# Kernel tuning notes

Hardware: AMD Instinct MI355X
Metric: run time of the kernel (lower is better)

## Reference

```python
import jax, jax.numpy as jnp
import numpy as np

H = 16  # num_heads
LN_EPS = 1e-5


def setup_inputs() -> dict:
    key = jax.random.key(0)
    ks = jax.random.split(key, 12)
    B, S, HS = 2, 1024, 1024
    D = HS // H
    vocab = 2 * 512 + 1  # 2*max_relative_position + 1
    inp = {
        "q": jax.random.normal(ks[0], (B, S, HS), jnp.float32),
        "k": jax.random.normal(ks[1], (B, S, HS), jnp.float32),
        "v": jax.random.normal(ks[2], (B, S, HS), jnp.float32),
        "rel_positions": jax.random.randint(ks[3], (S, S), 0, vocab, jnp.int64),
        "Wq": jax.random.normal(ks[4], (HS, HS), jnp.float32) * 0.02,
        "bq": jnp.zeros((HS,), jnp.float32),
        "Wk": jax.random.normal(ks[5], (HS, HS), jnp.float32) * 0.02,
        "bk": jnp.zeros((HS,), jnp.float32),
        "Wv": jax.random.normal(ks[6], (HS, HS), jnp.float32) * 0.02,
        "bv": jnp.zeros((HS,), jnp.float32),
        "rel_key_emb": jax.random.normal(ks[7], (vocab, D), jnp.float32) * 0.02,
        "rel_val_emb": jax.random.normal(ks[8], (vocab, D), jnp.float32) * 0.02,
        "Wo": jax.random.normal(ks[9], (HS, HS), jnp.float32) * 0.02,
        "bo": jnp.zeros((HS,), jnp.float32),
        "ln_g": jnp.ones((HS,), jnp.float32),
        "ln_b": jnp.zeros((HS,), jnp.float32),
    }
    return inp


def _layer_norm(x, g, b):
    mu = jnp.mean(x, axis=-1, keepdims=True)
    var = jnp.mean(jnp.square(x - mu), axis=-1, keepdims=True)
    return (x - mu) * jax.lax.rsqrt(var + LN_EPS) * g + b


def reference(q, k, v, rel_positions, Wq, bq, Wk, bk, Wv, bv,
              rel_key_emb, rel_val_emb, Wo, bo, ln_g, ln_b):
    B, S, HS = q.shape
    D = HS // H
    residual = q
    # projections (torch Linear: x @ W^T + b), split heads -> (B,H,S,D)
    qh = (q @ Wq.T + bq).reshape(B, S, H, D).transpose(0, 2, 1, 3)
    kh = (k @ Wk.T + bk).reshape(B, S, H, D).transpose(0, 2, 1, 3)
    vh = (v @ Wv.T + bv).reshape(B, S, H, D).transpose(0, 2, 1, 3)
    # relative embeddings: (S,S,D)
    rk = rel_key_emb[rel_positions]
    rv = rel_val_emb[rel_positions]
    # logits: content + relative-key term (note: original has NO 1/sqrt(d) scaling)
    logits = jnp.einsum('bhqd,bhkd->bhqk', qh, kh) \
           + jnp.einsum('bhqd,qkd->bhqk', qh, rk)
    weights = jax.nn.softmax(logits, axis=-1)
    # output: content + relative-value term
    ctx = jnp.einsum('bhqk,bhkd->bhqd', weights, vh) \
        + jnp.einsum('bhqk,qkd->bhqd', weights, rv)
    out = ctx.transpose(0, 2, 1, 3).reshape(B, S, HS) @ Wo.T + bo
    out = _layer_norm(out + residual, ln_g, ln_b)
    return (out, weights)
```

## Files before the change

kernel.cpp:

```cpp
#include <hip/hip_runtime.h>
#include <hip/hip_bf16.h>
#include <stdint.h>

#define B_   2
#define S_   1024
#define HS_  1024
#define H_   16
#define D_   64
#define V_   1025
#define VP_  1056
#define BH_  32
#define RTS_S 1072
#define RVS_  66

typedef __attribute__((ext_vector_type(8))) short  short8;
typedef __attribute__((ext_vector_type(4))) short  short4v;
typedef __attribute__((ext_vector_type(4))) float  floatx4;
typedef __attribute__((ext_vector_type(4))) int    intx4;
typedef __bf16 bf16x8 __attribute__((ext_vector_type(8)));

__device__ inline short f2b(float f) {
  union { float f; uint32_t u; } c; c.f = f;
  uint32_t u = c.u;
  uint32_t r = (u + 0x7fffu + ((u >> 16) & 1u)) >> 16;
  return (short)r;
}
__device__ inline float b2f(short s) {
  union { uint32_t u; float f; } c; c.u = ((uint32_t)(uint16_t)s) << 16;
  return c.f;
}
__device__ inline short8 cvt8(const float* p) {
  const floatx4* p4 = reinterpret_cast<const floatx4*>(p);
  floatx4 x = p4[0], y = p4[1];
  short8 r;
  r[0]=f2b(x[0]); r[1]=f2b(x[1]); r[2]=f2b(x[2]); r[3]=f2b(x[3]);
  r[4]=f2b(y[0]); r[5]=f2b(y[1]); r[6]=f2b(y[2]); r[7]=f2b(y[3]);
  return r;
}
__device__ inline short8 load_s8(const short* p) {
  return *reinterpret_cast<const short8*>(p);
}
__device__ inline floatx4 mfma16(short8 a, short8 b, floatx4 c) {
  return __builtin_amdgcn_mfma_f32_16x16x32_bf16(
      __builtin_bit_cast(bf16x8, a), __builtin_bit_cast(bf16x8, b), c, 0, 0, 0);
}

__global__ __launch_bounds__(256) void k_prep(const float* __restrict__ rve,
                                              const float* __restrict__ rke,
                                              short* __restrict__ rveB,
                                              short* __restrict__ rkeB) {
  int idx = blockIdx.x * 256 + threadIdx.x;
  if (idx < V_ * D_) {
    rveB[idx] = f2b(rve[idx]);
  } else {
    int j = idx - V_ * D_;
    if (j < V_ * D_) rkeB[j] = f2b(rke[j]);
  }
}

__global__ __launch_bounds__(256) void k_cvt(
    const float* __restrict__ q, const float* __restrict__ k, const float* __restrict__ v,
    const float* __restrict__ Wq, const float* __restrict__ Wk,
    const float* __restrict__ Wv, const float* __restrict__ Wo,
    short* __restrict__ xb, short* __restrict__ wb) {
  int z = blockIdx.z;
  const float* src = z == 0 ? q : z == 1 ? k : z == 2 ? v
                   : z == 3 ? Wq : z == 4 ? Wk : z == 5 ? Wv : Wo;
  int n = (z < 3) ? (1 << 21) : (1 << 20);
  short* dst = (z < 3) ? xb + (size_t)z * (1 << 21) : wb + (size_t)(z - 3) * (1 << 20);
  int i = (blockIdx.x * 256 + threadIdx.x) * 8;
  if (i < n) *reinterpret_cast<short8*>(&dst[i]) = cvt8(src + i);
}


__global__ __launch_bounds__(256, 4) void k_proj(
    const short* __restrict__ xb, const short* __restrict__ wb,
    const float* __restrict__ bq, const float* __restrict__ bk, const float* __restrict__ bv,
    short* __restrict__ qh, short* __restrict__ kh, short* __restrict__ vhT) {
  int which = blockIdx.z;
  const short* A  = xb + (size_t)which * (2048u * 1024u);
  const short* Bm = wb + (size_t)which * (1024u * 1024u);
  const float* bias = which == 0 ? bq : which == 1 ? bk : bv;
  int m0 = blockIdx.x * 64, n0 = blockIdx.y * 64;
  int tid = threadIdx.x, wid = tid >> 6, lane = tid & 63;
  int wr = wid >> 1, wc = wid & 1, qd = lane >> 4, c16 = lane & 15;
  __shared__ short As[4 * 64 * 8];
  __shared__ short Bs[4 * 64 * 8];
  int kk = tid & 3, rowi = tid >> 2;
  const short* ga = A  + (size_t)(m0 + rowi) * HS_ + kk * 8;
  const short* gb = Bm + (size_t)(n0 + rowi) * HS_ + kk * 8;
  floatx4 acc[2][2] = {};
  for (int k0 = 0; k0 < HS_; k0 += 32) {
    short8 av = load_s8(ga + k0);
    short8 bv8 = load_s8(gb + k0);
    __syncthreads();
    *reinterpret_cast<short8*>(&As[kk * 512 + rowi * 8]) = av;
    *reinterpret_cast<short8*>(&Bs[kk * 512 + rowi * 8]) = bv8;
    __syncthreads();
    short8 a0 = load_s8(&As[qd * 512 + (wr * 32 + c16) * 8]);
    short8 a1 = load_s8(&As[qd * 512 + (wr * 32 + 16 + c16) * 8]);
    short8 b0 = load_s8(&Bs[qd * 512 + (wc * 32 + c16) * 8]);
    short8 b1 = load_s8(&Bs[qd * 512 + (wc * 32 + 16 + c16) * 8]);
    acc[0][0] = mfma16(a0, b0, acc[0][0]);
    acc[0][1] = mfma16(a0, b1, acc[0][1]);
    acc[1][0] = mfma16(a1, b0, acc[1][0]);
    acc[1][1] = mfma16(a1, b1, acc[1][1]);
  }
#pragma unroll
  for (int mi = 0; mi < 2; mi++)
#pragma unroll
    for (int ni = 0; ni < 2; ni++) {
      int col = n0 + wc * 32 + ni * 16 + c16;
      float bs = bias[col];
      int gr0 = m0 + wr * 32 + mi * 16 + qd * 4;
      if (which < 2) {
        short* dst = which == 0 ? qh : kh;
#pragma unroll
        for (int r = 0; r < 4; r++)
          dst[(size_t)(gr0 + r) * HS_ + col] = f2b(acc[mi][ni][r] + bs);
      } else {
        int h = col >> 6, d = col & 63;
        int bb = gr0 >> 10, s = gr0 & 1023;
        short4v pk;
#pragma unroll
        for (int r = 0; r < 4; r++) pk[r] = f2b(acc[mi][ni][r] + bs);
        *reinterpret_cast<short4v*>(&vhT[(((size_t)(bb * H_ + h)) * D_ + d) * S_ + s]) = pk;
      }
    }
}

__global__ __launch_bounds__(256, 4) void k_score(
    const short* __restrict__ qh, const short* __restrict__ kh,
    const short* __restrict__ rkeB, const int* __restrict__ rp,
    float* __restrict__ weights) {
  int bh = blockIdx.y;
  int b = bh >> 4, h = bh & 15;
  int q0 = blockIdx.x * 16;
  int tid = threadIdx.x, wave = tid >> 6, lane = tid & 63;
  int qd = lane >> 4, c16 = lane & 15;
  __shared__ short Rt[16 * RTS_S];
  __shared__ float redA[4 * 16];
  __shared__ float redB[4 * 16];

  const short* aptr = qh + ((size_t)b * S_ + q0 + c16) * HS_ + h * 64 + qd * 8;
  short8 a0 = load_s8(aptr), a1 = load_s8(aptr + 32);

  for (int nt = wave; nt < VP_ / 16; nt += 4) {
    int p = nt * 16 + c16;
    short8 b0 = {}, b1 = {};
    if (p < V_) {
      b0 = load_s8(rkeB + (size_t)p * D_ + qd * 8);
      b1 = load_s8(rkeB + (size_t)p * D_ + 32 + qd * 8);
    }
    floatx4 acc = {};
    acc = mfma16(a0, b0, acc);
    acc = mfma16(a1, b1, acc);
#pragma unroll
    for (int r = 0; r < 4; r++) Rt[(qd * 4 + r) * RTS_S + p] = f2b(acc[r]);
  }
  __syncthreads();

  floatx4 acc[16];
  const int* rpq = rp + (size_t)q0 * S_;
#pragma unroll
  for (int it = 0; it < 16; it++) {
    int col = wave * 256 + it * 16 + c16;
    const short* bptr = kh + ((size_t)b * S_ + col) * HS_ + h * 64 + qd * 8;
    floatx4 a = {};
    a = mfma16(a0, load_s8(bptr), a);
    a = mfma16(a1, load_s8(bptr + 32), a);
#pragma unroll
    for (int r = 0; r < 4; r++) {
      int row = qd * 4 + r;
      int p = rpq[(size_t)row * S_ + col];
      a[r] += b2f(Rt[row * RTS_S + p]);
    }
    acc[it] = a;
  }

  float mx[4], inv[4];
#pragma unroll
  for (int r = 0; r < 4; r++) {
    float m = -1e30f;
#pragma unroll
    for (int it = 0; it < 16; it++) m = fmaxf(m, acc[it][r]);
#pragma unroll
    for (int off = 1; off < 16; off <<= 1) m = fmaxf(m, __shfl_xor(m, off));
    mx[r] = m;
    if (c16 == 0) redA[wave * 16 + qd * 4 + r] = m;
  }
  __syncthreads();
#pragma unroll
  for (int r = 0; r < 4; r++) {
    int row = qd * 4 + r;
    float m = fmaxf(fmaxf(redA[row], redA[16 + row]),
                    fmaxf(redA[32 + row], redA[48 + row]));
    mx[r] = m;
  }
  float sm[4] = {0.f, 0.f, 0.f, 0.f};
#pragma unroll
  for (int it = 0; it < 16; it++) {
#pragma unroll
    for (int r = 0; r < 4; r++) {
      float e = __expf(acc[it][r] - mx[r]);
      acc[it][r] = e;
      sm[r] += e;
    }
  }
#pragma unroll
  for (int r = 0; r < 4; r++) {
#pragma unroll
    for (int off = 1; off < 16; off <<= 1) sm[r] += __shfl_xor(sm[r], off);
    if (c16 == 0) redB[wave * 16 + qd * 4 + r] = sm[r];
  }
  __syncthreads();
#pragma unroll
  for (int r = 0; r < 4; r++) {
    int row = qd * 4 + r;
    inv[r] = 1.f / (redB[row] + redB[16 + row] + redB[32 + row] + redB[48 + row]);
  }

  float* wout = weights + (size_t)bh * S_ * S_ + (size_t)q0 * S_;
#pragma unroll
  for (int it = 0; it < 16; it++) {
    int col = wave * 256 + it * 16 + c16;
#pragma unroll
    for (int r = 0; r < 4; r++) {
      wout[(size_t)(qd * 4 + r) * S_ + col] = acc[it][r] * inv[r];
    }
  }
}

__global__ __launch_bounds__(256, 4) void k_relgemm(
    const float* __restrict__ weights, const int* __restrict__ rp,
    const short* __restrict__ rveB, float* __restrict__ ctx_rel) {
  int q = blockIdx.x;
  int tid = threadIdx.x, wave = tid >> 6, lane = tid & 63;
  int qd = lane >> 4, c16 = lane & 15;
  __shared__ int   rpl[S_];
  __shared__ short Wl[32][40];
  __shared__ short Rv[32][RVS_];

  {
    const intx4* r4 = reinterpret_cast<const intx4*>(rp + (size_t)q * S_);
    reinterpret_cast<intx4*>(rpl)[tid] = r4[tid];
  }
  __syncthreads();

  int sn = tid >> 3;
  int sk = (tid & 3) * 8;
  int part = tid & 7;
  const float* wbase = weights + ((size_t)sn * S_ + q) * S_;
  floatx4 acc0 = {}, acc1 = {};
  int d0 = wave * 16;

  for (int kc = 0; kc < S_; kc += 32) {
    {
      int skA = (tid & 7) * 4;
      floatx4 wv = *reinterpret_cast<const floatx4*>(wbase + kc + skA);
      short4v pk;
      pk[0] = f2b(wv[0]); pk[1] = f2b(wv[1]);
      pk[2] = f2b(wv[2]); pk[3] = f2b(wv[3]);
      *reinterpret_cast<short4v*>(&Wl[sn][skA]) = pk;
    }
    {
      int p = rpl[kc + sn];
      *reinterpret_cast<short8*>(&Rv[sn][part * 8]) =
          load_s8(rveB + (size_t)p * D_ + part * 8);
    }
    __syncthreads();
    short8 a0 = *reinterpret_cast<const short8*>(&Wl[c16][qd * 8]);
    short8 a1 = *reinterpret_cast<const short8*>(&Wl[16 + c16][qd * 8]);
    short8 bfr;
#pragma unroll
    for (int j = 0; j < 8; j++) bfr[j] = Rv[qd * 8 + j][d0 + c16];
    acc0 = mfma16(a0, bfr, acc0);
    acc1 = mfma16(a1, bfr, acc1);
    __syncthreads();
  }

  int dd = d0 + c16;
#pragma unroll
  for (int r = 0; r < 4; r++) {
    int bh0 = qd * 4 + r;
    ctx_rel[((size_t)0 * S_ + q) * HS_ + bh0 * 64 + dd] = acc0[r];
    ctx_rel[((size_t)1 * S_ + q) * HS_ + bh0 * 64 + dd] = acc1[r];
  }
}

__global__ __launch_bounds__(256, 4) void k_ctx2(
    const float* __restrict__ weights, const short* __restrict__ vhT,
    const float* __restrict__ ctx_rel, short* __restrict__ ctx) {
  int bh = blockIdx.y;
  int b = bh >> 4, h = bh & 15;
  int m0 = blockIdx.x * 64;
  int tid = threadIdx.x, wid = tid >> 6, lane = tid & 63;
  int wr = wid >> 1, wc = wid & 1, qd = lane >> 4, c16 = lane & 15;
  __shared__ short As[4 * 64 * 8];
  __shared__ short Bs[4 * 64 * 8];
  int kk = tid & 3, rowi = tid >> 2;
  const float* gaf = weights + (size_t)bh * S_ * S_ + (size_t)(m0 + rowi) * S_ + kk * 8;
  const short* gb  = vhT + ((size_t)bh * D_ + rowi) * S_ + kk * 8;
  floatx4 acc[2][2] = {};
  for (int k0 = 0; k0 < S_; k0 += 32) {
    short8 av = cvt8(gaf + k0);
    short8 bv8 = load_s8(gb + k0);
    __syncthreads();
    *reinterpret_cast<short8*>(&As[kk * 512 + rowi * 8]) = av;
    *reinterpret_cast<short8*>(&Bs[kk * 512 + rowi * 8]) = bv8;
    __syncthreads();
    short8 a0 = load_s8(&As[qd * 512 + (wr * 32 + c16) * 8]);
    short8 a1 = load_s8(&As[qd * 512 + (wr * 32 + 16 + c16) * 8]);
    short8 b0 = load_s8(&Bs[qd * 512 + (wc * 32 + c16) * 8]);
    short8 b1 = load_s8(&Bs[qd * 512 + (wc * 32 + 16 + c16) * 8]);
    acc[0][0] = mfma16(a0, b0, acc[0][0]);
    acc[0][1] = mfma16(a0, b1, acc[0][1]);
    acc[1][0] = mfma16(a1, b0, acc[1][0]);
    acc[1][1] = mfma16(a1, b1, acc[1][1]);
  }
#pragma unroll
  for (int mi = 0; mi < 2; mi++)
#pragma unroll
    for (int ni = 0; ni < 2; ni++) {
      int d = wc * 32 + ni * 16 + c16;
      int gq0 = m0 + wr * 32 + mi * 16 + qd * 4;
#pragma unroll
      for (int r = 0; r < 4; r++) {
        size_t off = ((size_t)b * S_ + gq0 + r) * HS_ + h * 64 + d;
        ctx[off] = f2b(acc[mi][ni][r] + ctx_rel[off]);
      }
    }
}

__global__ __launch_bounds__(256, 4) void k_oproj(
    const short* __restrict__ ctx, const short* __restrict__ wob,
    const float* __restrict__ bo, float* __restrict__ out0) {
  int m0 = blockIdx.x * 64, n0 = blockIdx.y * 64;
  int tid = threadIdx.x, wid = tid >> 6, lane = tid & 63;
  int wr = wid >> 1, wc = wid & 1, qd = lane >> 4, c16 = lane & 15;
  __shared__ short As[4 * 64 * 8];
  __shared__ short Bs[4 * 64 * 8];
  int kk = tid & 3, rowi = tid >> 2;
  const short* ga = ctx + (size_t)(m0 + rowi) * HS_ + kk * 8;
  const short* gb = wob + (size_t)(n0 + rowi) * HS_ + kk * 8;
  floatx4 acc[2][2] = {};
  for (int k0 = 0; k0 < HS_; k0 += 32) {
    short8 av = load_s8(ga + k0);
    short8 bv8 = load_s8(gb + k0);
    __syncthreads();
    *reinterpret_cast<short8*>(&As[kk * 512 + rowi * 8]) = av;
    *reinterpret_cast<short8*>(&Bs[kk * 512 + rowi * 8]) = bv8;
    __syncthreads();
    short8 a0 = load_s8(&As[qd * 512 + (wr * 32 + c16) * 8]);
    short8 a1 = load_s8(&As[qd * 512 + (wr * 32 + 16 + c16) * 8]);
    short8 b0 = load_s8(&Bs[qd * 512 + (wc * 32 + c16) * 8]);
    short8 b1 = load_s8(&Bs[qd * 512 + (wc * 32 + 16 + c16) * 8]);
    acc[0][0] = mfma16(a0, b0, acc[0][0]);
    acc[0][1] = mfma16(a0, b1, acc[0][1]);
    acc[1][0] = mfma16(a1, b0, acc[1][0]);
    acc[1][1] = mfma16(a1, b1, acc[1][1]);
  }
#pragma unroll
  for (int mi = 0; mi < 2; mi++)
#pragma unroll
    for (int ni = 0; ni < 2; ni++) {
      int col = n0 + wc * 32 + ni * 16 + c16;
      float bs = bo[col];
      int gr0 = m0 + wr * 32 + mi * 16 + qd * 4;
#pragma unroll
      for (int r = 0; r < 4; r++)
        out0[(size_t)(gr0 + r) * HS_ + col] = acc[mi][ni][r] + bs;
    }
}

__global__ __launch_bounds__(256) void k_ln(
    const float* __restrict__ out0, const float* __restrict__ resid,
    const float* __restrict__ g, const float* __restrict__ bb,
    float* __restrict__ out) {
  int row = blockIdx.x;
  int tid = threadIdx.x, wave = tid >> 6, lane = tid & 63;
  const floatx4* x4 = reinterpret_cast<const floatx4*>(out0 + (size_t)row * HS_);
  const floatx4* r4 = reinterpret_cast<const floatx4*>(resid + (size_t)row * HS_);
  floatx4 x = x4[tid] + r4[tid];
  float s = x[0] + x[1] + x[2] + x[3];
  float ss = x[0]*x[0] + x[1]*x[1] + x[2]*x[2] + x[3]*x[3];
  __shared__ float red[8];
#pragma unroll
  for (int off = 32; off > 0; off >>= 1) {
    s += __shfl_xor(s, off);
    ss += __shfl_xor(ss, off);
  }
  if (lane == 0) { red[wave] = s; red[wave + 4] = ss; }
  __syncthreads();
  s = red[0] + red[1] + red[2] + red[3];
  ss = red[4] + red[5] + red[6] + red[7];
  float mu = s * (1.f / 1024.f);
  float var = ss * (1.f / 1024.f) - mu * mu;
  float rs = rsqrtf(var + 1e-5f);
  int c = tid * 4;
  floatx4 gg = *reinterpret_cast<const floatx4*>(g + c);
  floatx4 bv = *reinterpret_cast<const floatx4*>(bb + c);
  floatx4 y = (x - mu) * rs * gg + bv;
  reinterpret_cast<floatx4*>(out + (size_t)row * HS_)[tid] = y;
}

extern "C" void kernel_launch(void* const* d_in, const int* in_sizes, int n_in,
                              void* d_out, int out_size, void* d_ws, size_t ws_size,
                              hipStream_t stream) {
  const float* q   = (const float*)d_in[0];
  const float* k   = (const float*)d_in[1];
  const float* v   = (const float*)d_in[2];
  const int*   rp  = (const int*)d_in[3];
  const float* Wq  = (const float*)d_in[4];
  const float* bq  = (const float*)d_in[5];
  const float* Wk  = (const float*)d_in[6];
  const float* bk  = (const float*)d_in[7];
  const float* Wv  = (const float*)d_in[8];
  const float* bv  = (const float*)d_in[9];
  const float* rke = (const float*)d_in[10];
  const float* rve = (const float*)d_in[11];
  const float* Wo  = (const float*)d_in[12];
  const float* bo  = (const float*)d_in[13];
  const float* lng = (const float*)d_in[14];
  const float* lnb = (const float*)d_in[15];

  float* out = (float*)d_out;
  float* weights = out + (size_t)B_ * S_ * HS_;

  char* ws = (char*)d_ws;
  short* qh      = (short*)(ws);
  short* kh      = (short*)(ws + 4194304);
  short* vhT     = (short*)(ws + 8388608);
  short* ctx     = (short*)(ws + 12582912);
  short* rveB    = (short*)(ws + 16777216);
  short* rkeB    = (short*)(ws + 16912384);
  float* ctx_rel = (float*)(ws + 17043968);
  float* out0    = (float*)(ws + 25432576);
  short* xb      = (short*)(ws + 33821184);
  short* wb      = (short*)(ws + 46404096);
  short* wob     = wb + (size_t)3 * (1 << 20);

  k_prep    <<<dim3(513),        256, 0, stream>>>(rve, rke, rveB, rkeB);
  k_cvt     <<<dim3(1024, 1, 7), 256, 0, stream>>>(q, k, v, Wq, Wk, Wv, Wo, xb, wb);
  k_proj    <<<dim3(32, 16, 3),  256, 0, stream>>>(xb, wb, bq, bk, bv, qh, kh, vhT);
  k_score   <<<dim3(64, 32),     256, 0, stream>>>(qh, kh, rkeB, rp, weights);
  k_relgemm <<<dim3(1024),       256, 0, stream>>>(weights, rp, rveB, ctx_rel);
  k_ctx2    <<<dim3(16, 32),     256, 0, stream>>>(weights, vhT, ctx_rel, ctx);
  k_oproj   <<<dim3(32, 16),     256, 0, stream>>>(ctx, wob, bo, out0);
  k_ln      <<<dim3(2048),       256, 0, stream>>>(out0, q, lng, lnb, out);
}
```

Baseline: 414.9 us.

## Fuse P·V content GEMM into score kernel and drop separate ctx kernel

The score kernel now writes the normalized bf16 probabilities into shared memory (reusing the relative-key table buffer) and immediately multiplies them by V, writing fp32 context to a workspace. The relative-value kernel then accumulates its term into that buffer with +=, and the output projection converts fp32 context to bf16 on load. This removes the k_ctx2 launch and its re-read of the full fp32 weights tensor from global memory. In exchange the score kernel does extra serial MFMA work per block, and the relgemm kernel performs read-modify-write on the context buffer.

```diff
diff --git a/kernel.cpp b/kernel.cpp
--- a/kernel.cpp
+++ b/kernel.cpp
@@ -10,8 +10,8 @@
 #define V_   1025
 #define VP_  1056
 #define BH_  32
-#define RTS_S 1072
-#define RVS_  66
+#define PTS_ 1096
+#define RVS_ 66
 
 typedef __attribute__((ext_vector_type(8))) short  short8;
 typedef __attribute__((ext_vector_type(4))) short  short4v;
@@ -71,7 +71,6 @@
   int i = (blockIdx.x * 256 + threadIdx.x) * 8;
   if (i < n) *reinterpret_cast<short8*>(&dst[i]) = cvt8(src + i);
 }
-
 
 __global__ __launch_bounds__(256, 4) void k_proj(
     const short* __restrict__ xb, const short* __restrict__ wb,
@@ -132,13 +131,14 @@
 __global__ __launch_bounds__(256, 4) void k_score(
     const short* __restrict__ qh, const short* __restrict__ kh,
     const short* __restrict__ rkeB, const int* __restrict__ rp,
-    float* __restrict__ weights) {
+    const short* __restrict__ vhT, float* __restrict__ weights,
+    float* __restrict__ ctxf) {
   int bh = blockIdx.y;
   int b = bh >> 4, h = bh & 15;
   int q0 = blockIdx.x * 16;
   int tid = threadIdx.x, wave = tid >> 6, lane = tid & 63;
   int qd = lane >> 4, c16 = lane & 15;
-  __shared__ short Rt[16 * RTS_S];
+  __shared__ short SH[16 * PTS_];
   __shared__ float redA[4 * 16];
   __shared__ float redB[4 * 16];
 
@@ -156,7 +156,7 @@
     acc = mfma16(a0, b0, acc);
     acc = mfma16(a1, b1, acc);
 #pragma unroll
-    for (int r = 0; r < 4; r++) Rt[(qd * 4 + r) * RTS_S + p] = f2b(acc[r]);
+    for (int r = 0; r < 4; r++) SH[(qd * 4 + r) * PTS_ + p] = f2b(acc[r]);
   }
   __syncthreads();
 
@@ -173,7 +173,7 @@
     for (int r = 0; r < 4; r++) {
       int row = qd * 4 + r;
       int p = rpq[(size_t)row * S_ + col];
-      a[r] += b2f(Rt[row * RTS_S + p]);
+      a[r] += b2f(SH[row * PTS_ + p]);
     }
     acc[it] = a;
   }
@@ -226,14 +226,31 @@
     int col = wave * 256 + it * 16 + c16;
 #pragma unroll
     for (int r = 0; r < 4; r++) {
-      wout[(size_t)(qd * 4 + r) * S_ + col] = acc[it][r] * inv[r];
-    }
+      int row = qd * 4 + r;
+      float w = acc[it][r] * inv[r];
+      wout[(size_t)row * S_ + col] = w;
+      SH[row * PTS_ + col] = f2b(w);
+    }
+  }
+  __syncthreads();
+
+  {
+    int d0 = wave * 16;
+    const short* vb = vhT + ((size_t)bh * D_ + d0 + c16) * S_ + qd * 8;
+    floatx4 apv = {};
+    for (int kc = 0; kc < S_; kc += 32) {
+      short8 pa = load_s8(&SH[c16 * PTS_ + kc + qd * 8]);
+      apv = mfma16(pa, load_s8(vb + kc), apv);
+    }
+    float* cf = ctxf + ((size_t)b * S_ + q0 + qd * 4) * HS_ + h * 64 + d0 + c16;
+#pragma unroll
+    for (int r = 0; r < 4; r++) cf[(size_t)r * HS_] = apv[r];
   }
 }
 
 __global__ __launch_bounds__(256, 4) void k_relgemm(
     const float* __restrict__ weights, const int* __restrict__ rp,
-    const short* __restrict__ rveB, float* __restrict__ ctx_rel) {
+    const short* __restrict__ rveB, float* __restrict__ ctxf) {
   int q = blockIdx.x;
   int tid = threadIdx.x, wave = tid >> 6, lane = tid & 63;
   int qd = lane >> 4, c16 = lane & 15;
@@ -248,7 +265,6 @@
   __syncthreads();
 
   int sn = tid >> 3;
-  int sk = (tid & 3) * 8;
   int part = tid & 7;
   const float* wbase = weights + ((size_t)sn * S_ + q) * S_;
   floatx4 acc0 = {}, acc1 = {};
@@ -283,57 +299,15 @@
 #pragma unroll
   for (int r = 0; r < 4; r++) {
     int bh0 = qd * 4 + r;
-    ctx_rel[((size_t)0 * S_ + q) * HS_ + bh0 * 64 + dd] = acc0[r];
-    ctx_rel[((size_t)1 * S_ + q) * HS_ + bh0 * 64 + dd] = acc1[r];
-  }
-}
-
-__global__ __launch_bounds__(256, 4) void k_ctx2(
-    const float* __restrict__ weights, const short* __restrict__ vhT,
-    const float* __restrict__ ctx_rel, short* __restrict__ ctx) {
-  int bh = blockIdx.y;
-  int b = bh >> 4, h = bh & 15;
-  int m0 = blockIdx.x * 64;
-  int tid = threadIdx.x, wid = tid >> 6, lane = tid & 63;
-  int wr = wid >> 1, wc = wid & 1, qd = lane >> 4, c16 = lane & 15;
-  __shared__ short As[4 * 64 * 8];
-  __shared__ short Bs[4 * 64 * 8];
-  int kk = tid & 3, rowi = tid >> 2;
-  const float* gaf = weights + (size_t)bh * S_ * S_ + (size_t)(m0 + rowi) * S_ + kk * 8;
-  const short* gb  = vhT + ((size_t)bh * D_ + rowi) * S_ + kk * 8;
-  floatx4 acc[2][2] = {};
-  for (int k0 = 0; k0 < S_; k0 += 32) {
-    short8 av = cvt8(gaf + k0);
-    short8 bv8 = load_s8(gb + k0);
-    __syncthreads();
-    *reinterpret_cast<short8*>(&As[kk * 512 + rowi * 8]) = av;
-    *reinterpret_cast<short8*>(&Bs[kk * 512 + rowi * 8]) = bv8;
-    __syncthreads();
-    short8 a0 = load_s8(&As[qd * 512 + (wr * 32 + c16) * 8]);
-    short8 a1 = load_s8(&As[qd * 512 + (wr * 32 + 16 + c16) * 8]);
-    short8 b0 = load_s8(&Bs[qd * 512 + (wc * 32 + c16) * 8]);
-    short8 b1 = load_s8(&Bs[qd * 512 + (wc * 32 + 16 + c16) * 8]);
-    acc[0][0] = mfma16(a0, b0, acc[0][0]);
-    acc[0][1] = mfma16(a0, b1, acc[0][1]);
-    acc[1][0] = mfma16(a1, b0, acc[1][0]);
-    acc[1][1] = mfma16(a1, b1, acc[1][1]);
-  }
-#pragma unroll
-  for (int mi = 0; mi < 2; mi++)
-#pragma unroll
-    for (int ni = 0; ni < 2; ni++) {
-      int d = wc * 32 + ni * 16 + c16;
-      int gq0 = m0 + wr * 32 + mi * 16 + qd * 4;
-#pragma unroll
-      for (int r = 0; r < 4; r++) {
-        size_t off = ((size_t)b * S_ + gq0 + r) * HS_ + h * 64 + d;
-        ctx[off] = f2b(acc[mi][ni][r] + ctx_rel[off]);
-      }
-    }
+    size_t o0 = ((size_t)0 * S_ + q) * HS_ + bh0 * 64 + dd;
+    size_t o1 = ((size_t)1 * S_ + q) * HS_ + bh0 * 64 + dd;
+    ctxf[o0] += acc0[r];
+    ctxf[o1] += acc1[r];
+  }
 }
 
 __global__ __launch_bounds__(256, 4) void k_oproj(
-    const short* __restrict__ ctx, const short* __restrict__ wob,
+    const float* __restrict__ ctxf, const short* __restrict__ wob,
     const float* __restrict__ bo, float* __restrict__ out0) {
   int m0 = blockIdx.x * 64, n0 = blockIdx.y * 64;
   int tid = threadIdx.x, wid = tid >> 6, lane = tid & 63;
@@ -341,11 +315,11 @@
   __shared__ short As[4 * 64 * 8];
   __shared__ short Bs[4 * 64 * 8];
   int kk = tid & 3, rowi = tid >> 2;
-  const short* ga = ctx + (size_t)(m0 + rowi) * HS_ + kk * 8;
+  const float* ga = ctxf + (size_t)(m0 + rowi) * HS_ + kk * 8;
   const short* gb = wob + (size_t)(n0 + rowi) * HS_ + kk * 8;
   floatx4 acc[2][2] = {};
   for (int k0 = 0; k0 < HS_; k0 += 32) {
-    short8 av = load_s8(ga + k0);
+    short8 av = cvt8(ga + k0);
     short8 bv8 = load_s8(gb + k0);
     __syncthreads();
     *reinterpret_cast<short8*>(&As[kk * 512 + rowi * 8]) = av;
@@ -431,10 +405,9 @@
   short* qh      = (short*)(ws);
   short* kh      = (short*)(ws + 4194304);
   short* vhT     = (short*)(ws + 8388608);
-  short* ctx     = (short*)(ws + 12582912);
   short* rveB    = (short*)(ws + 16777216);
   short* rkeB    = (short*)(ws + 16912384);
-  float* ctx_rel = (float*)(ws + 17043968);
+  float* ctxf    = (float*)(ws + 17043968);
   float* out0    = (float*)(ws + 25432576);
   short* xb      = (short*)(ws + 33821184);
   short* wb      = (short*)(ws + 46404096);
@@ -443,9 +416,8 @@
   k_prep    <<<dim3(513),        256, 0, stream>>>(rve, rke, rveB, rkeB);
   k_cvt     <<<dim3(1024, 1, 7), 256, 0, stream>>>(q, k, v, Wq, Wk, Wv, Wo, xb, wb);
   k_proj    <<<dim3(32, 16, 3),  256, 0, stream>>>(xb, wb, bq, bk, bv, qh, kh, vhT);
-  k_score   <<<dim3(64, 32),     256, 0, stream>>>(qh, kh, rkeB, rp, weights);
-  k_relgemm <<<dim3(1024),       256, 0, stream>>>(weights, rp, rveB, ctx_rel);
-  k_ctx2    <<<dim3(16, 32),     256, 0, stream>>>(weights, vhT, ctx_rel, ctx);
-  k_oproj   <<<dim3(32, 16),     256, 0, stream>>>(ctx, wob, bo, out0);
+  k_score   <<<dim3(64, 32),     256, 0, stream>>>(qh, kh, rkeB, rp, vhT, weights, ctxf);
+  k_relgemm <<<dim3(1024),       256, 0, stream>>>(weights, rp, rveB, ctxf);
+  k_oproj   <<<dim3(32, 16),     256, 0, stream>>>(ctxf, wob, bo, out0);
   k_ln      <<<dim3(2048),       256, 0, stream>>>(out0, q, lng, lnb, out);
 }
```

Measured after the change: 386.0 us. 1.07x faster.
